# Performance work log

Measured on AMD Instinct MI355X. Metric: run time of the kernel, lower is better.

Reference implementation:

```python
import jax, jax.numpy as jnp
import numpy as np

N_NODES = 50000
N_EDGES = 600000
N_FEAT = 256
N_HID = 128
N_CLASS = 64
HEADS = 8
LEAKY_SLOPE = 0.2


def setup_inputs() -> dict:
    key = jax.random.key(0)
    ks = jax.random.split(key, 12)
    D0 = N_HID // HEADS  # 16 per-head dim, layer 0
    x = jax.random.normal(ks[0], (N_NODES, N_FEAT), dtype=jnp.float32)
    edge_index = jax.random.randint(ks[1], (2, N_EDGES), 0, N_NODES, dtype=jnp.int64)
    s0 = 1.0 / np.sqrt(N_FEAT)
    s1 = 1.0 / np.sqrt(N_HID)
    return {
        "x": x,
        "edge_index": edge_index,
        "W0": jax.random.normal(ks[2], (N_FEAT, HEADS * D0), dtype=jnp.float32) * s0,
        "a_src0": jax.random.normal(ks[3], (HEADS, D0), dtype=jnp.float32) * s0,
        "a_dst0": jax.random.normal(ks[4], (HEADS, D0), dtype=jnp.float32) * s0,
        "b0": jnp.zeros((HEADS * D0,), dtype=jnp.float32),
        "W1": jax.random.normal(ks[5], (N_HID, HEADS * N_CLASS), dtype=jnp.float32) * s1,
        "a_src1": jax.random.normal(ks[6], (HEADS, N_CLASS), dtype=jnp.float32) * s1,
        "a_dst1": jax.random.normal(ks[7], (HEADS, N_CLASS), dtype=jnp.float32) * s1,
        "b1": jnp.zeros((N_CLASS,), dtype=jnp.float32),
    }


def gat_conv(x, src, dst, W, a_s, a_d, b, concat, num_nodes):
    H, D = a_s.shape
    h = (x @ W).reshape(-1, H, D)                    # [N, H, D]
    alpha_s = jnp.einsum('nhd,hd->nh', h, a_s)       # [N, H]
    alpha_d = jnp.einsum('nhd,hd->nh', h, a_d)       # [N, H]
    e = jax.nn.leaky_relu(alpha_s[src] + alpha_d[dst], LEAKY_SLOPE)  # [E, H]
    # numerically stable edge-softmax grouped by destination node
    m = jax.ops.segment_max(e, dst, num_segments=num_nodes)
    m = jnp.where(jnp.isfinite(m), m, 0.0)           # nodes with no in-edges
    ex = jnp.exp(e - m[dst])
    denom = jax.ops.segment_sum(ex, dst, num_segments=num_nodes)
    alpha = ex / (denom[dst] + 1e-16)                # [E, H]
    msg = h[src] * alpha[:, :, None]                 # [E, H, D]
    out = jax.ops.segment_sum(msg, dst, num_segments=num_nodes)  # [N, H, D]
    if concat:
        out = out.reshape(num_nodes, H * D)
    else:
        out = out.mean(axis=1)
    return out + b


def reference(x, edge_index, W0, a_src0, a_dst0, b0, W1, a_src1, a_dst1, b1):
    src, dst = edge_index[0], edge_index[1]
    h = gat_conv(x, src, dst, W0, a_src0, a_dst0, b0, True, N_NODES)
    h = jax.nn.elu(h)  # eval mode: dropout is identity
    h = gat_conv(h, src, dst, W1, a_src1, a_dst1, b1, False, N_NODES)
    return jax.nn.log_softmax(h, axis=-1)
```

## Files before the change

### kernel.cpp

```cpp
#include <hip/hip_runtime.h>
#include <hip/hip_bf16.h>
#include <math.h>

#define NN 50000
#define NE 600000
#define NF 256
#define NHID 128
#define HEADS 8
#define D0 16
#define NCLS 64
#define NB1 196

#define PK0 (9 * 8 * 64 * 8)
#define PK1 (4 * 32 * 64 * 8)
#define PKA (4 * 64 * 8)
#define CASTN (NN * NF / 4)
#define PREPN (PK0 + PK1 + PKA)

typedef __attribute__((ext_vector_type(8))) short short8;
typedef __attribute__((ext_vector_type(4))) float floatx4;

__device__ __forceinline__ float bf16lo(uint v) { return __uint_as_float((v & 0xffffu) << 16); }
__device__ __forceinline__ float bf16hi(uint v) { return __uint_as_float(v & 0xffff0000u); }
__device__ __forceinline__ uint packbf16(float a, float b) {
    return (uint)__bfloat16_as_ushort(__float2bfloat16(a)) |
           ((uint)__bfloat16_as_ushort(__float2bfloat16(b)) << 16);
}
__device__ __forceinline__ short f2bf(float v) {
    return (short)__bfloat16_as_ushort(__float2bfloat16(v));
}
__device__ __forceinline__ float readlanef(float v, int l) {
    return __int_as_float(__builtin_amdgcn_readlane(__float_as_int(v), l));
}


__global__ void scan1_kernel(const int* __restrict__ deg, int* __restrict__ rs,
                             int* __restrict__ bsum) {
    __shared__ int sh[256];
    int tid = threadIdx.x;
    int i = blockIdx.x * 256 + tid;
    int v = (i < NN) ? deg[i] : 0;
    sh[tid] = v;
    __syncthreads();
    for (int off = 1; off < 256; off <<= 1) {
        int t = (tid >= off) ? sh[tid - off] : 0;
        __syncthreads();
        sh[tid] += t;
        __syncthreads();
    }
    if (i < NN) rs[i] = sh[tid] - v;
    if (tid == 255) bsum[blockIdx.x] = sh[255];
}

__global__ void scan2_kernel(const int* __restrict__ bsum, int* __restrict__ bsumx) {
    __shared__ int sh[256];
    int tid = threadIdx.x;
    int v = (tid < NB1) ? bsum[tid] : 0;
    sh[tid] = v;
    __syncthreads();
    for (int off = 1; off < 256; off <<= 1) {
        int t = (tid >= off) ? sh[tid - off] : 0;
        __syncthreads();
        sh[tid] += t;
        __syncthreads();
    }
    if (tid < NB1) bsumx[tid] = sh[tid] - v;
}

__global__ void scan3_kernel(int* __restrict__ rs, const int* __restrict__ bsumx) {
    int i = blockIdx.x * 256 + threadIdx.x;
    if (i < NN) rs[i] += bsumx[i >> 8];
}

__global__ void scatter_kernel(const int* __restrict__ ei, const int* __restrict__ rs,
                               int* __restrict__ cnt2, int* __restrict__ csr) {
    int e = blockIdx.x * 256 + threadIdx.x;
    if (e >= NE) return;
    int s = ei[e], d = ei[NE + e];
    int pos = rs[d] + atomicAdd(&cnt2[d], 1);
    csr[pos] = s;
}


__global__ void fused_prep_kernel(const float* __restrict__ x, short* __restrict__ xb,
                                  const int* __restrict__ ei, int* __restrict__ deg,
                                  const float* __restrict__ W0, const float* __restrict__ aS0,
                                  const float* __restrict__ aD0, const float* __restrict__ W1,
                                  const float* __restrict__ aS1, const float* __restrict__ aD1,
                                  short* __restrict__ Bp0, short* __restrict__ Bp1,
                                  short* __restrict__ wA1b) {
    int i = blockIdx.x * 256 + threadIdx.x;
    if (i < CASTN) {
        float4 v = ((const float4*)x)[i];
        short4 r;
        r.x = f2bf(v.x); r.y = f2bf(v.y); r.z = f2bf(v.z); r.w = f2bf(v.w);
        ((short4*)xb)[i] = r;
        return;
    }
    int e = i - CASTN;
    if (e < NE) {
        atomicAdd(&deg[ei[NE + e]], 1);
        return;
    }
    int tid = e - NE;
    if (tid < PK0) {
        int j = tid & 7, l = (tid >> 3) & 63, ks = (tid >> 9) & 7, t = tid >> 12;
        int k = ks * 32 + (l >> 4) * 8 + j;
        float v;
        if (t < 8) {
            int c = t * 16 + (l & 15);
            v = W0[(size_t)k * 128 + c];
        } else {
            int jj = l & 15;
            int hh = jj & 7;
            const float* av = (jj < 8) ? aS0 : aD0;
            float sum = 0.f;
            for (int dd = 0; dd < D0; ++dd)
                sum += W0[(size_t)k * 128 + hh * D0 + dd] * av[hh * D0 + dd];
            v = sum;
        }
        Bp0[tid] = f2bf(v);
    } else if (tid < PK0 + PK1) {
        int t2 = tid - PK0;
        int j = t2 & 7, l = (t2 >> 3) & 63, ks = (t2 >> 9) & 31, t = t2 >> 14;
        int kk = ks * 32 + (l >> 4) * 8 + j;
        int c = t * 16 + (l & 15);
        Bp1[t2] = f2bf(W1[(size_t)(kk & 127) * 512 + (kk >> 7) * 64 + c] * 0.125f);
    } else if (tid < PREPN) {
        int t3 = tid - PK0 - PK1;
        int j = t3 & 7, l = (t3 >> 3) & 63, ks = t3 >> 9;
        int k = ks * 32 + (l >> 4) * 8 + j;
        int c = l & 15;
        int h = c & 7;
        const float* av = (c < 8) ? aS1 : aD1;
        float sum = 0.f;
        for (int d2 = 0; d2 < NCLS; ++d2)
            sum += W1[(size_t)k * 512 + h * NCLS + d2] * av[h * NCLS + d2];
        wA1b[t3] = f2bf(sum);
    }
}


__global__ __launch_bounds__(256) void gemm0_mfma(const short* __restrict__ xb,
                                                  const short* __restrict__ Bp,
                                                  ushort* __restrict__ h0b,
                                                  float* __restrict__ as0,
                                                  float* __restrict__ ad0) {
    int lane = threadIdx.x & 63, wave = threadIdx.x >> 6;
    int rg = wave >> 1, cg = wave & 1;
    int q = lane >> 4, c16 = lane & 15;
    int row0 = blockIdx.x * 32 + rg * 16;
    int arow = row0 + c16;
    if (arow > NN - 1) arow = NN - 1;
    const short* ap = xb + (size_t)arow * NF + q * 8;
    floatx4 acc[5] = {};
#pragma unroll
    for (int ks = 0; ks < 8; ++ks) {
        short8 af = *(const short8*)(ap + ks * 32);
#pragma unroll
        for (int tt = 0; tt < 4; ++tt) {
            int t = cg * 4 + tt;
            short8 bf = *(const short8*)(Bp + (((size_t)t * 8 + ks) * 64 + lane) * 8);
            acc[tt] = __builtin_amdgcn_mfma_f32_16x16x32_bf16(af, bf, acc[tt], 0, 0, 0);
        }
        if (cg) {
            short8 bf = *(const short8*)(Bp + (((size_t)8 * 8 + ks) * 64 + lane) * 8);
            acc[4] = __builtin_amdgcn_mfma_f32_16x16x32_bf16(af, bf, acc[4], 0, 0, 0);
        }
    }
#pragma unroll
    for (int r = 0; r < 4; ++r) {
        int grow = row0 + q * 4 + r;
        if (grow >= NN) continue;
#pragma unroll
        for (int tt = 0; tt < 4; ++tt)
            h0b[(size_t)grow * NHID + cg * 64 + tt * 16 + c16] =
                (ushort)f2bf(acc[tt][r]);
        if (cg) {
            float v = acc[4][r];
            if (c16 < 8) as0[grow * 8 + c16] = v;
            else         ad0[grow * 8 + (c16 - 8)] = v;
        }
    }
}

__global__ __launch_bounds__(256) void alpha1_mfma(const ushort* __restrict__ x1b,
                                                   const short* __restrict__ wA1b,
                                                   float* __restrict__ as1,
                                                   float* __restrict__ ad1) {
    int lane = threadIdx.x & 63, wave = threadIdx.x >> 6;
    int q = lane >> 4, c16 = lane & 15;
    int row0 = blockIdx.x * 64 + wave * 16;
    int arow = row0 + c16;
    if (arow > NN - 1) arow = NN - 1;
    const short* ap = (const short*)x1b + (size_t)arow * NHID + q * 8;
    floatx4 acc = {};
#pragma unroll
    for (int ks = 0; ks < 4; ++ks) {
        short8 af = *(const short8*)(ap + ks * 32);
        short8 bf = *(const short8*)(wA1b + (((size_t)ks) * 64 + lane) * 8);
        acc = __builtin_amdgcn_mfma_f32_16x16x32_bf16(af, bf, acc, 0, 0, 0);
    }
#pragma unroll
    for (int r = 0; r < 4; ++r) {
        int grow = row0 + q * 4 + r;
        if (grow >= NN) continue;
        float v = acc[r];
        if (c16 < 8) as1[grow * 8 + c16] = v;
        else         ad1[grow * 8 + (c16 - 8)] = v;
    }
}

__global__ __launch_bounds__(256) void gemm1_mfma(const short* __restrict__ AGG,
                                                  const short* __restrict__ Bp,
                                                  const float* __restrict__ b1,
                                                  float* __restrict__ out) {
    int lane = threadIdx.x & 63, wave = threadIdx.x >> 6;
    int q = lane >> 4, c16 = lane & 15;
    int row0 = blockIdx.x * 64 + wave * 16;
    int arow = row0 + c16;
    if (arow > NN - 1) arow = NN - 1;
    const short* ap = AGG + (size_t)arow * 1024 + q * 8;
    floatx4 acc[4] = {};
    for (int ks = 0; ks < 32; ++ks) {
        short8 af = *(const short8*)(ap + ks * 32);
#pragma unroll
        for (int t = 0; t < 4; ++t) {
            short8 bf = *(const short8*)(Bp + (((size_t)t * 32 + ks) * 64 + lane) * 8);
            acc[t] = __builtin_amdgcn_mfma_f32_16x16x32_bf16(af, bf, acc[t], 0, 0, 0);
        }
    }
    float bias[4];
#pragma unroll
    for (int t = 0; t < 4; ++t) bias[t] = b1[t * 16 + c16];
#pragma unroll
    for (int r = 0; r < 4; ++r) {
        int grow = row0 + q * 4 + r;
        float z[4];
        float mx = -INFINITY;
#pragma unroll
        for (int t = 0; t < 4; ++t) {
            z[t] = acc[t][r] + bias[t];
            mx = fmaxf(mx, z[t]);
        }
        mx = fmaxf(mx, __shfl_xor(mx, 1));
        mx = fmaxf(mx, __shfl_xor(mx, 2));
        mx = fmaxf(mx, __shfl_xor(mx, 4));
        mx = fmaxf(mx, __shfl_xor(mx, 8));
        float s = 0.f;
#pragma unroll
        for (int t = 0; t < 4; ++t) s += expf(z[t] - mx);
        s += __shfl_xor(s, 1);
        s += __shfl_xor(s, 2);
        s += __shfl_xor(s, 4);
        s += __shfl_xor(s, 8);
        float lse = mx + logf(s);
        if (grow < NN) {
#pragma unroll
            for (int t = 0; t < 4; ++t)
                out[(size_t)grow * NCLS + t * 16 + c16] = z[t] - lse;
        }
    }
}


__global__ __launch_bounds__(256) void fused_edge0(
    const int* __restrict__ rs, const int* __restrict__ deg, const int* __restrict__ csr,
    const ushort* __restrict__ h0b, const float* __restrict__ as0, const float* __restrict__ ad0,
    const float* __restrict__ b0, ushort* __restrict__ x1b) {
    int d = (blockIdx.x * 256 + threadIdx.x) >> 6;
    int lane = threadIdx.x & 63;
    if (d >= NN) return;
    int row = rs[d], dg = deg[d];
    int hl = lane & 7, g = lane >> 3;
    int hp = lane >> 3;
    float adv = ad0[d * 8 + hl];
    float den = 0.f;
    float2 acc = {0.f, 0.f};
    for (int base = 0; base < dg; base += 8) {
        int i = base + g;
        int s = (i < dg) ? csr[row + i] : 0;
        float ev = as0[s * 8 + hl] + adv;
        ev = ev > 0.f ? ev : 0.2f * ev;
        float p = (i < dg) ? __expf(ev) : 0.f;
        den += p;
        uint vbuf[8];
#pragma unroll
        for (int g2 = 0; g2 < 8; ++g2) {
            int sg = __builtin_amdgcn_readlane(s, g2 * 8);
            vbuf[g2] = *(const uint*)(h0b + (size_t)sg * NHID + 2 * lane);
        }
#pragma unroll
        for (int g2 = 0; g2 < 8; ++g2) {
            float ph = __shfl(p, g2 * 8 + hp);
            acc.x += bf16lo(vbuf[g2]) * ph;
            acc.y += bf16hi(vbuf[g2]) * ph;
        }
    }
    den += __shfl_xor(den, 8);
    den += __shfl_xor(den, 16);
    den += __shfl_xor(den, 32);
    float dh = __shfl(den, hp);
    float inv = 1.f / (dh + 1e-16f);
    float2 bb = ((const float2*)b0)[lane];
    float o0 = acc.x * inv + bb.x;
    float o1 = acc.y * inv + bb.y;
    o0 = o0 > 0.f ? o0 : expf(o0) - 1.f;
    o1 = o1 > 0.f ? o1 : expf(o1) - 1.f;
    *(uint*)(x1b + (size_t)d * NHID + 2 * lane) = packbf16(o0, o1);
}

__global__ __launch_bounds__(256) void fused_edge1(
    const int* __restrict__ rs, const int* __restrict__ deg, const int* __restrict__ csr,
    const ushort* __restrict__ x1b, const float* __restrict__ as1, const float* __restrict__ ad1,
    ushort* __restrict__ AGG) {
    int gw = (blockIdx.x * 256 + threadIdx.x) >> 6;
    int d = gw >> 1;
    int w = gw & 1;
    int lane = threadIdx.x & 63;
    if (d >= NN) return;
    int row = rs[d], dg = deg[d];
    int hh = lane & 3, eslot = lane >> 2;
    float adv = ad1[d * 8 + w * 4 + hh];
    float den = 0.f;
    float2 acc[4] = {};
    for (int base = 0; base < dg; base += 16) {
        int i = base + eslot;
        int s = (i < dg) ? csr[row + i] : 0;
        float ev = as1[s * 8 + w * 4 + hh] + adv;
        ev = ev > 0.f ? ev : 0.2f * ev;
        float p = (i < dg) ? __expf(ev) : 0.f;
        den += p;
        uint vbuf[16];
#pragma unroll
        for (int g2 = 0; g2 < 16; ++g2) {
            int sg = __builtin_amdgcn_readlane(s, g2 * 4);
            vbuf[g2] = *(const uint*)(x1b + (size_t)sg * NHID + 2 * lane);
        }
#pragma unroll
        for (int g2 = 0; g2 < 16; ++g2) {
            float2 xv = {bf16lo(vbuf[g2]), bf16hi(vbuf[g2])};
#pragma unroll
            for (int h = 0; h < 4; ++h) {
                float ph = readlanef(p, g2 * 4 + h);
                acc[h].x += xv.x * ph;
                acc[h].y += xv.y * ph;
            }
        }
    }
    den += __shfl_xor(den, 4);
    den += __shfl_xor(den, 8);
    den += __shfl_xor(den, 16);
    den += __shfl_xor(den, 32);
#pragma unroll
    for (int h = 0; h < 4; ++h) {
        float dh = readlanef(den, h);
        float inv = 1.f / (dh + 1e-16f);
        *(uint*)(AGG + (size_t)d * 1024 + (w * 4 + h) * NHID + 2 * lane) =
            packbf16(acc[h].x * inv, acc[h].y * inv);
    }
}


extern "C" void kernel_launch(void* const* d_in, const int* in_sizes, int n_in,
                              void* d_out, int out_size, void* d_ws, size_t ws_size,
                              hipStream_t stream) {
    const float* x   = (const float*)d_in[0];
    const int*   ei  = (const int*)d_in[1];
    const float* W0  = (const float*)d_in[2];
    const float* aS0 = (const float*)d_in[3];
    const float* aD0 = (const float*)d_in[4];
    const float* b0  = (const float*)d_in[5];
    const float* W1  = (const float*)d_in[6];
    const float* aS1 = (const float*)d_in[7];
    const float* aD1 = (const float*)d_in[8];
    const float* b1  = (const float*)d_in[9];
    float* out = (float*)d_out;

    char* ws = (char*)d_ws;
    ushort* x1b = (ushort*)ws; ws += (size_t)NN * NHID * 2;
    ushort* h0b = (ushort*)ws; ws += (size_t)NN * NHID * 2;
    ushort* AGG = (ushort*)ws; ws += (size_t)NN * 1024 * 2;
    short* xb   = (short*)ws; ws += (size_t)NN * NF * 2;
    float* as0  = (float*)ws; ws += (size_t)NN * HEADS * 4;
    float* ad0  = (float*)ws; ws += (size_t)NN * HEADS * 4;
    float* as1  = (float*)ws; ws += (size_t)NN * HEADS * 4;
    float* ad1  = (float*)ws; ws += (size_t)NN * HEADS * 4;
    short* Bp0  = (short*)ws; ws += (size_t)PK0 * 2;
    short* Bp1  = (short*)ws; ws += (size_t)PK1 * 2;
    short* wA1b = (short*)ws; ws += (size_t)PKA * 2;
    int* deg    = (int*)ws; ws += (size_t)NN * 4;
    int* cnt2   = (int*)ws; ws += (size_t)NN * 4;
    int* rs     = (int*)ws; ws += (size_t)NN * 4;
    int* bsum   = (int*)ws; ws += 256 * 4;
    int* bsumx  = (int*)ws; ws += 256 * 4;
    int* csr    = (int*)ws; ws += (size_t)NE * 4;

    const int FUSEDN = CASTN + NE + PREPN;

    hipMemsetAsync(deg, 0, (size_t)2 * NN * 4, stream);
    fused_prep_kernel<<<(FUSEDN + 255) / 256, 256, 0, stream>>>(
        x, xb, ei, deg, W0, aS0, aD0, W1, aS1, aD1, Bp0, Bp1, wA1b);

    scan1_kernel<<<NB1, 256, 0, stream>>>(deg, rs, bsum);
    scan2_kernel<<<1, 256, 0, stream>>>(bsum, bsumx);
    scan3_kernel<<<NB1, 256, 0, stream>>>(rs, bsumx);
    scatter_kernel<<<(NE + 255) / 256, 256, 0, stream>>>(ei, rs, cnt2, csr);

    gemm0_mfma<<<(NN + 31) / 32, 256, 0, stream>>>(xb, Bp0, h0b, as0, ad0);
    fused_edge0<<<(NN + 3) / 4, 256, 0, stream>>>(rs, deg, csr, h0b, as0, ad0, b0, x1b);

    alpha1_mfma<<<(NN + 63) / 64, 256, 0, stream>>>(x1b, wA1b, as1, ad1);
    fused_edge1<<<(2 * NN + 3) / 4, 256, 0, stream>>>(rs, deg, csr, x1b, as1, ad1, AGG);
    gemm1_mfma<<<(NN + 63) / 64, 256, 0, stream>>>((const short*)AGG, Bp1, b1, out);
}
```

Measured before the change: 329.2 us.

## Compute layer-1 edge aggregation with MFMA, two destination nodes per wave

The layer-1 weighted neighbor aggregation now runs on MFMA 16x16x32 bf16 instructions instead of scalar FMAs fed by readlane broadcasts. Each wave handles two destination nodes, with attention weights packed as the A operand (heads by edges) and gathered neighbor features as the B operand. This is meant to cut the VALU and readlane cost of the per-head accumulation. In exchange, attention weights are rounded to bf16 before accumulation and the denominator, the gathers become scattered 16-bit loads, the AGG stores are 16-bit scattered writes, and lanes idle when the two nodes' degrees differ.

```diff
diff --git a/kernel.cpp b/kernel.cpp
--- a/kernel.cpp
+++ b/kernel.cpp
@@ -29,8 +29,8 @@
 __device__ __forceinline__ short f2bf(float v) {
     return (short)__bfloat16_as_ushort(__float2bfloat16(v));
 }
-__device__ __forceinline__ float readlanef(float v, int l) {
-    return __int_as_float(__builtin_amdgcn_readlane(__float_as_int(v), l));
+__device__ __forceinline__ float bf16tof(short v) {
+    return __uint_as_float(((uint)(ushort)v) << 16);
 }
 
 
@@ -315,49 +315,58 @@
     const ushort* __restrict__ x1b, const float* __restrict__ as1, const float* __restrict__ ad1,
     ushort* __restrict__ AGG) {
     int gw = (blockIdx.x * 256 + threadIdx.x) >> 6;
-    int d = gw >> 1;
-    int w = gw & 1;
     int lane = threadIdx.x & 63;
-    if (d >= NN) return;
-    int row = rs[d], dg = deg[d];
-    int hh = lane & 3, eslot = lane >> 2;
-    float adv = ad1[d * 8 + w * 4 + hh];
+    int dA = 2 * gw;
+    if (dA >= NN) return;
+    int dB = dA + 1;
+    int q = lane >> 4, c16 = lane & 15, h7 = lane & 7;
+    int d_l = (lane >= 32) ? dB : dA;
+    int row_l = rs[d_l], dg_l = deg[d_l];
+    bool V = ((lane & 8) == 0) == (lane < 32);
+    float adv = ad1[d_l * 8 + h7];
+    int dgA = __shfl(dg_l, 0);
+    int dgB = __shfl(dg_l, 32);
+    int dgmax = dgA > dgB ? dgA : dgB;
     float den = 0.f;
-    float2 acc[4] = {};
-    for (int base = 0; base < dg; base += 16) {
-        int i = base + eslot;
-        int s = (i < dg) ? csr[row + i] : 0;
-        float ev = as1[s * 8 + w * 4 + hh] + adv;
-        ev = ev > 0.f ? ev : 0.2f * ev;
-        float p = (i < dg) ? __expf(ev) : 0.f;
-        den += p;
-        uint vbuf[16];
-#pragma unroll
-        for (int g2 = 0; g2 < 16; ++g2) {
-            int sg = __builtin_amdgcn_readlane(s, g2 * 4);
-            vbuf[g2] = *(const uint*)(x1b + (size_t)sg * NHID + 2 * lane);
-        }
-#pragma unroll
-        for (int g2 = 0; g2 < 16; ++g2) {
-            float2 xv = {bf16lo(vbuf[g2]), bf16hi(vbuf[g2])};
-#pragma unroll
-            for (int h = 0; h < 4; ++h) {
-                float ph = readlanef(p, g2 * 4 + h);
-                acc[h].x += xv.x * ph;
-                acc[h].y += xv.y * ph;
-            }
-        }
-    }
-    den += __shfl_xor(den, 4);
+    floatx4 acc[8] = {};
+    for (int base = 0; base < dgmax; base += 16) {
+        short8 af;
+        int sarr[8];
+#pragma unroll
+        for (int j = 0; j < 8; ++j) {
+            int idx = base + (q & 1) * 8 + j;
+            int s = 0;
+            if (idx < dg_l) s = csr[row_l + idx];
+            sarr[j] = s;
+            float ev = as1[s * 8 + h7] + adv;
+            ev = ev > 0.f ? ev : 0.2f * ev;
+            float p = __expf(ev);
+            p = (idx < dg_l && V) ? p : 0.f;
+            short pb = f2bf(p);
+            af[j] = pb;
+            den += bf16tof(pb);
+        }
+#pragma unroll
+        for (int t = 0; t < 8; ++t) {
+            short8 bv;
+#pragma unroll
+            for (int j = 0; j < 8; ++j)
+                bv[j] = (short)x1b[(size_t)sarr[j] * NHID + t * 16 + c16];
+            acc[t] = __builtin_amdgcn_mfma_f32_16x16x32_bf16(af, bv, acc[t], 0, 0, 0);
+        }
+    }
     den += __shfl_xor(den, 8);
     den += __shfl_xor(den, 16);
-    den += __shfl_xor(den, 32);
-#pragma unroll
-    for (int h = 0; h < 4; ++h) {
-        float dh = readlanef(den, h);
+    int hbase = (q & 1) * 4;
+#pragma unroll
+    for (int r = 0; r < 4; ++r) {
+        int hh = hbase + r;
+        float dh = __shfl(den, (lane & 32) + hh);
         float inv = 1.f / (dh + 1e-16f);
-        *(uint*)(AGG + (size_t)d * 1024 + (w * 4 + h) * NHID + 2 * lane) =
-            packbf16(acc[h].x * inv, acc[h].y * inv);
+        size_t base_a = (size_t)d_l * 1024 + (size_t)hh * 128 + c16;
+#pragma unroll
+        for (int t = 0; t < 8; ++t)
+            AGG[base_a + t * 16] = (ushort)f2bf(acc[t][r] * inv);
     }
 }
 
@@ -411,6 +420,6 @@
     fused_edge0<<<(NN + 3) / 4, 256, 0, stream>>>(rs, deg, csr, h0b, as0, ad0, b0, x1b);
 
     alpha1_mfma<<<(NN + 63) / 64, 256, 0, stream>>>(x1b, wA1b, as1, ad1);
-    fused_edge1<<<(2 * NN + 3) / 4, 256, 0, stream>>>(rs, deg, csr, x1b, as1, ad1, AGG);
+    fused_edge1<<<(NN / 2 + 3) / 4, 256, 0, stream>>>(rs, deg, csr, x1b, as1, ad1, AGG);
     gemm1_mfma<<<(NN + 63) / 64, 256, 0, stream>>>((const short*)AGG, Bp1, b1, out);
 }
```

After: 325.6 us. About the same (-1.1%).
